# Kernel tuning notes

Measured on AMD Instinct MI355X. Metric: run time of the kernel, lower is better.

Reference implementation:

```python
import jax, jax.numpy as jnp
import numpy as np

B, S, E, D = 4, 2048, 1024, 512


def setup_inputs() -> dict:
    key = jax.random.key(0)
    ks = jax.random.split(key, 7)
    s_in = 1.0 / np.sqrt(E)
    return {
        "x": jax.random.normal(ks[0], (B, S, E), dtype=jnp.float32),
        "wq": jax.random.uniform(ks[1], (E, D), jnp.float32, -s_in, s_in),
        "bq": jax.random.uniform(ks[2], (D,), jnp.float32, -s_in, s_in),
        "wk": jax.random.uniform(ks[3], (E, D), jnp.float32, -s_in, s_in),
        "bk": jax.random.uniform(ks[4], (D,), jnp.float32, -s_in, s_in),
        "wv": jax.random.uniform(ks[5], (E, D), jnp.float32, -s_in, s_in),
        "bv": jax.random.uniform(ks[6], (D,), jnp.float32, -s_in, s_in),
    }


def reference(x, wq, bq, wk, bk, wv, bv):
    # QKV projections: [B,S,E] @ [E,D] -> [B,S,D]
    q = jnp.einsum('bse,ed->bsd', x, wq) + bq
    k = jnp.einsum('bse,ed->bsd', x, wk) + bk
    v = jnp.einsum('bse,ed->bsd', x, wv) + bv
    # scores [B,S,S]
    scores = jnp.einsum('bqd,bkd->bqk', q, k)
    # causal mask applied before scaling (as in original; -inf unaffected by scale)
    causal = jnp.tril(jnp.ones((S, S), dtype=bool))
    scores = jnp.where(causal[None], scores, -jnp.inf)
    scores = scores / jnp.sqrt(jnp.float32(D))
    attn = jax.nn.softmax(scores, axis=-1)
    return jnp.einsum('bqk,bkd->bqd', attn, v)
```

## Files before the change

### kernel.cpp

```cpp
#include <hip/hip_runtime.h>
#include <math.h>


typedef __attribute__((ext_vector_type(4))) float f32x4;
typedef __attribute__((ext_vector_type(16))) float f32x16;
typedef __attribute__((ext_vector_type(8))) short bf16x8;
typedef __attribute__((ext_vector_type(8))) unsigned short u16x8;

#define B_ 4
#define S_ 2048
#define E_ 1024
#define D_ 512

__device__ __forceinline__ unsigned short f2bf(float f) {
  unsigned u = __float_as_uint(f);
  u += 0x7fffu + ((u >> 16) & 1u);
  return (unsigned short)(u >> 16);
}

__device__ __forceinline__ float bf2f(unsigned short h) {
  return __uint_as_float(((unsigned)h) << 16);
}

template<int N> __device__ __forceinline__ void wait_vm() {
  if constexpr (N == 0)      asm volatile("s_waitcnt vmcnt(0)" ::: "memory");
  else if constexpr (N == 3) asm volatile("s_waitcnt vmcnt(3)" ::: "memory");
  else if constexpr (N == 4) asm volatile("s_waitcnt vmcnt(4)" ::: "memory");
  else if constexpr (N == 6) asm volatile("s_waitcnt vmcnt(6)" ::: "memory");
  else static_assert(N != N, "unsupported vmcnt");
}


template<int ROWS, int NTHR>
__device__ __forceinline__ void stage_tile32(const unsigned short* __restrict__ g, long ld,
                                             long rowBase, int kBase,
                                             unsigned short* lds, int tid) {
  constexpr int CALLS = (ROWS * 64) / (NTHR * 16);
  #pragma unroll
  for (int i = 0; i < CALLS; ++i) {
    int idx = i * NTHR + tid;
    int row = idx >> 2, cc = idx & 3;
    int src_g = cc ^ ((row >> 1) & 3);
    __builtin_amdgcn_global_load_lds(
      (const __attribute__((address_space(1))) void*)(g + (rowBase + row) * ld + kBase + src_g * 8),
      (__attribute__((address_space(3))) void*)(lds + idx * 8),
      16, 0, 0);
  }
}

template<int MT, int NTT>
__device__ __forceinline__ void compute_tile32(const unsigned short* As, const unsigned short* Bs,
                                               int a_row0, int b_row0, int lane,
                                               f32x16 (&acc)[MT][NTT]) {
  int lr = lane & 31, lhalf = lane >> 5;
  int p = (lr >> 1) & 3;
  #pragma unroll
  for (int ki = 0; ki < 2; ++ki) {
    int slot = ((ki * 2 + lhalf) ^ p) * 8;
    bf16x8 af[MT], bf[NTT];
    #pragma unroll
    for (int mt = 0; mt < MT; ++mt)
      af[mt] = *(const bf16x8*)(As + (a_row0 + mt * 32 + lr) * 32 + slot);
    #pragma unroll
    for (int nt = 0; nt < NTT; ++nt)
      bf[nt] = *(const bf16x8*)(Bs + (b_row0 + nt * 32 + lr) * 32 + slot);
    #pragma unroll
    for (int mt = 0; mt < MT; ++mt)
      #pragma unroll
      for (int nt = 0; nt < NTT; ++nt)
        acc[mt][nt] = __builtin_amdgcn_mfma_f32_32x32x16_bf16(af[mt], bf[nt], acc[mt][nt], 0, 0, 0);
  }
}

template<int AROWS, int BROWS, int NTHR, int MT, int NTT>
__device__ __forceinline__ void mainloop32(
    const unsigned short* __restrict__ A, long lda, long rowA,
    const unsigned short* __restrict__ Bt, long ldb, long rowB,
    int nsteps, unsigned short* AsBuf, unsigned short* BsBuf,
    int tid, int lane, int a_row0, int b_row0, f32x16 (&acc)[MT][NTT]) {
  constexpr int ASZ = AROWS * 32, BSZ = BROWS * 32;
  constexpr int LPS = (AROWS * 64) / (NTHR * 16) + (BROWS * 64) / (NTHR * 16);
  unsigned short *a0 = AsBuf, *a1 = AsBuf + ASZ, *a2 = AsBuf + 2 * ASZ;
  unsigned short *b0 = BsBuf, *b1 = BsBuf + BSZ, *b2 = BsBuf + 2 * BSZ;
  stage_tile32<AROWS, NTHR>(A, lda, rowA, 0, a0, tid);
  stage_tile32<BROWS, NTHR>(Bt, ldb, rowB, 0, b0, tid);
  if (nsteps > 1) {
    stage_tile32<AROWS, NTHR>(A, lda, rowA, 32, a1, tid);
    stage_tile32<BROWS, NTHR>(Bt, ldb, rowB, 32, b1, tid);
  }
  for (int t = 0; t < nsteps; ++t) {
    if (t < nsteps - 1) wait_vm<LPS>(); else wait_vm<0>();
    __builtin_amdgcn_s_barrier();
    __builtin_amdgcn_sched_barrier(0);
    compute_tile32<MT, NTT>(a0, b0, a_row0, b_row0, lane, acc);
    if (t + 2 < nsteps) {
      stage_tile32<AROWS, NTHR>(A, lda, rowA, (t + 2) * 32, a2, tid);
      stage_tile32<BROWS, NTHR>(Bt, ldb, rowB, (t + 2) * 32, b2, tid);
    }
    unsigned short* ta = a0; a0 = a1; a1 = a2; a2 = ta;
    unsigned short* tb = b0; b0 = b1; b1 = b2; b2 = tb;
  }
}


template<int ROWS, int NTHR>
__device__ __forceinline__ void stage_tile64(const unsigned short* __restrict__ g, long ld,
                                             long rowBase, int kBase,
                                             unsigned short* lds, int tid) {
  constexpr int CALLS = (ROWS * 128) / (NTHR * 16);
  #pragma unroll
  for (int i = 0; i < CALLS; ++i) {
    int idx = i * NTHR + tid;
    int row = idx >> 3, cc = idx & 7;
    int src_g = cc ^ (row & 7);
    __builtin_amdgcn_global_load_lds(
      (const __attribute__((address_space(1))) void*)(g + (rowBase + row) * ld + kBase + src_g * 8),
      (__attribute__((address_space(3))) void*)(lds + idx * 8),
      16, 0, 0);
  }
}

__device__ __forceinline__ void compute_pv64(const unsigned short* As, const unsigned short* Bs,
                                             int a_row0, int b_row0, int lane, bf16x8 ones,
                                             f32x16 (&acc)[2], f32x16& accl) {
  int lr = lane & 31, lhalf = lane >> 5;
  int p = lr & 7;
  #pragma unroll
  for (int ki = 0; ki < 4; ++ki) {
    int slot = ((ki * 2 + lhalf) ^ p) * 8;
    bf16x8 af  = *(const bf16x8*)(As + (a_row0 + lr) * 64 + slot);
    bf16x8 bf0 = *(const bf16x8*)(Bs + (b_row0 + lr) * 64 + slot);
    bf16x8 bf1 = *(const bf16x8*)(Bs + (b_row0 + 32 + lr) * 64 + slot);
    accl   = __builtin_amdgcn_mfma_f32_32x32x16_bf16(af, ones, accl, 0, 0, 0);
    acc[0] = __builtin_amdgcn_mfma_f32_32x32x16_bf16(af, bf0, acc[0], 0, 0, 0);
    acc[1] = __builtin_amdgcn_mfma_f32_32x32x16_bf16(af, bf1, acc[1], 0, 0, 0);
  }
}

__device__ __forceinline__ void pv_mainloop64(
    const unsigned short* __restrict__ A, long rowA,
    const unsigned short* __restrict__ Bt, long rowB,
    int nsteps, unsigned short (*As)[64 * 64], unsigned short (*Bs)[128 * 64],
    int tid, int lane, int a_row0, int b_row0,
    f32x16 (&acc)[2], f32x16& accl) {
  bf16x8 ones;
  #pragma unroll
  for (int j = 0; j < 8; ++j) ones[j] = (short)0x3F80;
  stage_tile64<64, 256>(A, S_, rowA, 0, As[0], tid);
  stage_tile64<128, 256>(Bt, S_, rowB, 0, Bs[0], tid);
  if (nsteps > 1) {
    stage_tile64<64, 256>(A, S_, rowA, 64, As[1], tid);
    stage_tile64<128, 256>(Bt, S_, rowB, 64, Bs[1], tid);
  }
  int cur = 0;
  for (int t = 0; t < nsteps; ++t) {
    if (t < nsteps - 1) wait_vm<6>(); else wait_vm<0>();
    __builtin_amdgcn_s_barrier();
    __builtin_amdgcn_sched_barrier(0);
    compute_pv64(As[cur], Bs[cur], a_row0, b_row0, lane, ones, acc, accl);
    if (t + 2 < nsteps) {
      int nxt = (cur + 2) % 3;
      stage_tile64<64, 256>(A, S_, rowA, (t + 2) * 64, As[nxt], tid);
      stage_tile64<128, 256>(Bt, S_, rowB, (t + 2) * 64, Bs[nxt], tid);
    }
    cur = (cur + 1) % 3;
  }
}


__global__ __launch_bounds__(256) void convert_f32_bf16(const float* __restrict__ src,
                                                        unsigned short* __restrict__ dst) {
  long i = (long)blockIdx.x * 256 + threadIdx.x;
  f32x4 a = ((const f32x4*)src)[2 * i];
  f32x4 b = ((const f32x4*)src)[2 * i + 1];
  u16x8 o;
  #pragma unroll
  for (int j = 0; j < 4; ++j) { o[j] = f2bf(a[j]); o[4 + j] = f2bf(b[j]); }
  ((u16x8*)dst)[i] = o;
}

__global__ __launch_bounds__(256) void build_wT(const float* __restrict__ wq,
                                                const float* __restrict__ wk,
                                                const float* __restrict__ wv,
                                                unsigned short* __restrict__ wbT) {
  int o = blockIdx.x * 256 + threadIdx.x;
  int n = o >> 10, k = o & 1023;
  const float* w = (n < 512) ? wq : ((n < 1024) ? wk : wv);
  int d = n & 511;
  wbT[o] = f2bf(w[(long)k * 512 + d]);
}

__global__ __launch_bounds__(256, 3) void qkv_gemm(
    const unsigned short* __restrict__ xb, const unsigned short* __restrict__ wbT,
    const float* __restrict__ bq, const float* __restrict__ bk, const float* __restrict__ bv,
    unsigned short* __restrict__ qb, unsigned short* __restrict__ kb,
    unsigned short* __restrict__ vb) {
  __shared__ unsigned short As[3][128 * 32], Bs[3][128 * 32];
  int tid = threadIdx.x, wave = tid >> 6, lane = tid & 63;
  int wm = wave >> 1, wn = wave & 1;
  int wg = blockIdx.x;
  int swz = (wg & 7) * 96 + (wg >> 3);
  int nb = swz % 12, mb = swz / 12;
  long rowA = (long)mb * 128, rowB = (long)nb * 128;
  f32x16 acc[2][2] = {};
  mainloop32<128, 128, 256, 2, 2>(xb, E_, rowA, wbT, E_, rowB, E_ / 32,
                                  &As[0][0], &Bs[0][0], tid, lane, wm * 64, wn * 64, acc);
  int lc = lane & 31, lhi = (lane >> 5) * 4;
  #pragma unroll
  for (int nt = 0; nt < 2; ++nt) {
    int n = (int)rowB + wn * 64 + nt * 32 + lc;
    int d = n & 511;
    float bias; unsigned short* dst;
    if (n < 512)       { bias = bq[d]; dst = qb; }
    else if (n < 1024) { bias = bk[d]; dst = kb; }
    else               { bias = bv[d]; dst = vb; }
    #pragma unroll
    for (int mt = 0; mt < 2; ++mt) {
      long mbase = rowA + wm * 64 + mt * 32 + lhi;
      #pragma unroll
      for (int r = 0; r < 16; ++r) {
        long m = mbase + (r & 3) + 8 * (r >> 2);
        dst[m * D_ + d] = f2bf(acc[mt][nt][r] + bias);
      }
    }
  }
}

__global__ __launch_bounds__(256) void transpose_v(const unsigned short* __restrict__ vb,
                                                   unsigned short* __restrict__ vtb) {
  int dblk = blockIdx.x;
  int sblk = blockIdx.y;
  int b = blockIdx.z;
  __shared__ unsigned short ls[64][72];
  int tid = threadIdx.x;
  int r = tid >> 3, c8 = (tid & 7) * 8;
  long d0 = (long)dblk * 64, s0 = (long)sblk * 64;
  #pragma unroll
  for (int p = 0; p < 2; ++p) {
    u16x8 v = *(const u16x8*)(vb + ((long)b * S_ + s0 + r + p * 32) * D_ + d0 + c8);
    *(u16x8*)&ls[r + p * 32][c8] = v;
  }
  __syncthreads();
  #pragma unroll
  for (int p = 0; p < 2; ++p) {
    int d = r + p * 32;
    u16x8 o;
    #pragma unroll
    for (int j = 0; j < 8; ++j) o[j] = ls[c8 + j][d];
    *(u16x8*)(vtb + ((long)b * D_ + d0 + d) * S_ + s0 + c8) = o;
  }
}

__global__ __launch_bounds__(256, 4) void scores_gemm(
    const unsigned short* __restrict__ qb, const unsigned short* __restrict__ kb,
    unsigned short* __restrict__ sc) {
  int jb = blockIdx.x, im = 31 - blockIdx.y, b = blockIdx.z;
  if (2 * jb > im) return;
  __shared__ unsigned short As[3][64 * 32], Bs[3][128 * 32];
  int tid = threadIdx.x, wave = tid >> 6, lane = tid & 63;
  int wm = wave >> 1, wn = wave & 1;
  const unsigned short* A  = qb + (long)b * S_ * D_;
  const unsigned short* Bt = kb + (long)b * S_ * D_;
  long rowA = (long)im * 64, rowB = (long)jb * 128;
  f32x16 acc[1][2] = {};
  mainloop32<64, 128, 256, 1, 2>(A, D_, rowA, Bt, D_, rowB, D_ / 32,
                                 &As[0][0], &Bs[0][0], tid, lane, wm * 32, wn * 64, acc);
  unsigned short* po = sc + (long)b * S_ * S_;
  const float cexp = 1.4426950408889634f / 22.627416997969522f;
  int lc = lane & 31, lhi = (lane >> 5) * 4;
  long mbase = rowA + wm * 32 + lhi;
  #pragma unroll
  for (int r = 0; r < 16; ++r) {
    long m = mbase + (r & 3) + 8 * (r >> 2);
    #pragma unroll
    for (int nt = 0; nt < 2; ++nt) {
      long n = rowB + wn * 64 + nt * 32 + lc;
      float p = (n <= m) ? exp2f(acc[0][nt][r] * cexp) : 0.f;
      po[m * S_ + n] = f2bf(p);
    }
  }
}

__global__ __launch_bounds__(256, 2) void pv_gemm(
    const unsigned short* __restrict__ sc, const unsigned short* __restrict__ vtb,
    float* __restrict__ out) {
  int bn = blockIdx.x, bm = 31 - blockIdx.y, b = blockIdx.z;
  __shared__ unsigned short As[3][64 * 64], Bs[3][128 * 64];
  int tid = threadIdx.x, wave = tid >> 6, lane = tid & 63;
  int wm = wave >> 1, wn = wave & 1;
  const unsigned short* A  = sc  + (long)b * S_ * S_;
  const unsigned short* Bt = vtb + (long)b * D_ * S_;
  long rowA = (long)bm * 64, rowB = (long)bn * 128;
  int nsteps = bm + 1;
  f32x16 acc[2] = {};
  f32x16 accl = {};
  pv_mainloop64(A, rowA, Bt, rowB, nsteps, As, Bs, tid, lane,
                wm * 32, wn * 64, acc, accl);
  float* oo = out + (long)b * S_ * D_;
  int lc = lane & 31, lhi = (lane >> 5) * 4;
  long mbase = rowA + wm * 32 + lhi;
  #pragma unroll
  for (int r = 0; r < 16; ++r) {
    long m = mbase + (r & 3) + 8 * (r >> 2);
    float inv = 1.f / accl[r];
    #pragma unroll
    for (int nt = 0; nt < 2; ++nt) {
      long n = rowB + wn * 64 + nt * 32 + lc;
      oo[m * D_ + n] = acc[nt][r] * inv;
    }
  }
}

extern "C" void kernel_launch(void* const* d_in, const int* in_sizes, int n_in,
                              void* d_out, int out_size, void* d_ws, size_t ws_size,
                              hipStream_t stream) {
  const float* x   = (const float*)d_in[0];
  const float* wq  = (const float*)d_in[1];
  const float* bq  = (const float*)d_in[2];
  const float* wk  = (const float*)d_in[3];
  const float* bk  = (const float*)d_in[4];
  const float* wv  = (const float*)d_in[5];
  const float* bv  = (const float*)d_in[6];
  float* out = (float*)d_out;

  char* ws = (char*)d_ws;
  unsigned short* xb  = (unsigned short*)(ws);
  unsigned short* wbT = (unsigned short*)(ws + 16777216);
  unsigned short* qb  = (unsigned short*)(ws + 19922944);
  unsigned short* kb  = (unsigned short*)(ws + 28311552);
  unsigned short* vb  = (unsigned short*)(ws + 36700160);
  unsigned short* vtb = (unsigned short*)(ws + 45088768);
  unsigned short* sc  = (unsigned short*)(ws + 53477376);

  convert_f32_bf16<<<dim3(4096), dim3(256), 0, stream>>>(x, xb);
  build_wT<<<dim3(6144), dim3(256), 0, stream>>>(wq, wk, wv, wbT);
  qkv_gemm<<<dim3(768), dim3(256), 0, stream>>>(xb, wbT, bq, bk, bv, qb, kb, vb);
  transpose_v<<<dim3(8, 32, 4), dim3(256), 0, stream>>>(vb, vtb);
  scores_gemm<<<dim3(16, 32, 4), dim3(256), 0, stream>>>(qb, kb, sc);
  pv_gemm<<<dim3(4, 32, 4), dim3(256), 0, stream>>>(sc, vtb, out);
}
```

Baseline: 115.9 us.

## Fuse input conversions into one kernel and V transpose into QKV GEMM epilogue

Merges the x bf16 conversion and the weight transpose-convert into a single prep launch. The V-projection blocks of the QKV GEMM now write their tile transposed through LDS straight into the V^T buffer, so the separate transpose kernel and the intermediate V buffer go away. This saves two launches and one full read/write pass over V, at the cost of an extra LDS staging step and barriers in the V epilogue.

```diff
diff --git a/kernel.cpp b/kernel.cpp
--- a/kernel.cpp
+++ b/kernel.cpp
@@ -168,34 +168,38 @@
 }
 
 
-__global__ __launch_bounds__(256) void convert_f32_bf16(const float* __restrict__ src,
-                                                        unsigned short* __restrict__ dst) {
-  long i = (long)blockIdx.x * 256 + threadIdx.x;
-  f32x4 a = ((const f32x4*)src)[2 * i];
-  f32x4 b = ((const f32x4*)src)[2 * i + 1];
-  u16x8 o;
-  #pragma unroll
-  for (int j = 0; j < 4; ++j) { o[j] = f2bf(a[j]); o[4 + j] = f2bf(b[j]); }
-  ((u16x8*)dst)[i] = o;
-}
-
-__global__ __launch_bounds__(256) void build_wT(const float* __restrict__ wq,
-                                                const float* __restrict__ wk,
-                                                const float* __restrict__ wv,
-                                                unsigned short* __restrict__ wbT) {
-  int o = blockIdx.x * 256 + threadIdx.x;
-  int n = o >> 10, k = o & 1023;
-  const float* w = (n < 512) ? wq : ((n < 1024) ? wk : wv);
-  int d = n & 511;
-  wbT[o] = f2bf(w[(long)k * 512 + d]);
+__global__ __launch_bounds__(256) void prep(const float* __restrict__ x,
+                                            const float* __restrict__ wq,
+                                            const float* __restrict__ wk,
+                                            const float* __restrict__ wv,
+                                            unsigned short* __restrict__ xb,
+                                            unsigned short* __restrict__ wbT) {
+  int bx = blockIdx.x;
+  if (bx < 4096) {
+    long i = (long)bx * 256 + threadIdx.x;
+    f32x4 a = ((const f32x4*)x)[2 * i];
+    f32x4 b = ((const f32x4*)x)[2 * i + 1];
+    u16x8 o;
+    #pragma unroll
+    for (int j = 0; j < 4; ++j) { o[j] = f2bf(a[j]); o[4 + j] = f2bf(b[j]); }
+    ((u16x8*)xb)[i] = o;
+  } else {
+    int o = (bx - 4096) * 256 + threadIdx.x;
+    int n = o >> 10, k = o & 1023;
+    const float* w = (n < 512) ? wq : ((n < 1024) ? wk : wv);
+    int d = n & 511;
+    wbT[o] = f2bf(w[(long)k * 512 + d]);
+  }
 }
 
 __global__ __launch_bounds__(256, 3) void qkv_gemm(
     const unsigned short* __restrict__ xb, const unsigned short* __restrict__ wbT,
     const float* __restrict__ bq, const float* __restrict__ bk, const float* __restrict__ bv,
     unsigned short* __restrict__ qb, unsigned short* __restrict__ kb,
-    unsigned short* __restrict__ vb) {
-  __shared__ unsigned short As[3][128 * 32], Bs[3][128 * 32];
+    unsigned short* __restrict__ vtb) {
+  __shared__ unsigned short lds[24576];
+  unsigned short* AsB = lds;
+  unsigned short* BsB = lds + 3 * 4096;
   int tid = threadIdx.x, wave = tid >> 6, lane = tid & 63;
   int wm = wave >> 1, wn = wave & 1;
   int wg = blockIdx.x;
@@ -204,50 +208,51 @@
   long rowA = (long)mb * 128, rowB = (long)nb * 128;
   f32x16 acc[2][2] = {};
   mainloop32<128, 128, 256, 2, 2>(xb, E_, rowA, wbT, E_, rowB, E_ / 32,
-                                  &As[0][0], &Bs[0][0], tid, lane, wm * 64, wn * 64, acc);
+                                  AsB, BsB, tid, lane, wm * 64, wn * 64, acc);
   int lc = lane & 31, lhi = (lane >> 5) * 4;
-  #pragma unroll
-  for (int nt = 0; nt < 2; ++nt) {
-    int n = (int)rowB + wn * 64 + nt * 32 + lc;
-    int d = n & 511;
-    float bias; unsigned short* dst;
-    if (n < 512)       { bias = bq[d]; dst = qb; }
-    else if (n < 1024) { bias = bk[d]; dst = kb; }
-    else               { bias = bv[d]; dst = vb; }
-    #pragma unroll
-    for (int mt = 0; mt < 2; ++mt) {
-      long mbase = rowA + wm * 64 + mt * 32 + lhi;
+  if (rowB < 1024) {
+    #pragma unroll
+    for (int nt = 0; nt < 2; ++nt) {
+      int n = (int)rowB + wn * 64 + nt * 32 + lc;
+      int d = n & 511;
+      float bias; unsigned short* dst;
+      if (n < 512) { bias = bq[d]; dst = qb; }
+      else         { bias = bk[d]; dst = kb; }
       #pragma unroll
-      for (int r = 0; r < 16; ++r) {
-        long m = mbase + (r & 3) + 8 * (r >> 2);
-        dst[m * D_ + d] = f2bf(acc[mt][nt][r] + bias);
+      for (int mt = 0; mt < 2; ++mt) {
+        long mbase = rowA + wm * 64 + mt * 32 + lhi;
+        #pragma unroll
+        for (int r = 0; r < 16; ++r) {
+          long m = mbase + (r & 3) + 8 * (r >> 2);
+          dst[m * D_ + d] = f2bf(acc[mt][nt][r] + bias);
+        }
       }
     }
-  }
-}
-
-__global__ __launch_bounds__(256) void transpose_v(const unsigned short* __restrict__ vb,
-                                                   unsigned short* __restrict__ vtb) {
-  int dblk = blockIdx.x;
-  int sblk = blockIdx.y;
-  int b = blockIdx.z;
-  __shared__ unsigned short ls[64][72];
-  int tid = threadIdx.x;
-  int r = tid >> 3, c8 = (tid & 7) * 8;
-  long d0 = (long)dblk * 64, s0 = (long)sblk * 64;
-  #pragma unroll
-  for (int p = 0; p < 2; ++p) {
-    u16x8 v = *(const u16x8*)(vb + ((long)b * S_ + s0 + r + p * 32) * D_ + d0 + c8);
-    *(u16x8*)&ls[r + p * 32][c8] = v;
-  }
-  __syncthreads();
-  #pragma unroll
-  for (int p = 0; p < 2; ++p) {
-    int d = r + p * 32;
-    u16x8 o;
-    #pragma unroll
-    for (int j = 0; j < 8; ++j) o[j] = ls[c8 + j][d];
-    *(u16x8*)(vtb + ((long)b * D_ + d0 + d) * S_ + s0 + c8) = o;
+  } else {
+    __syncthreads();
+    #pragma unroll
+    for (int nt = 0; nt < 2; ++nt) {
+      int n_loc = wn * 64 + nt * 32 + lc;
+      float bias = bv[(int)(rowB - 1024) + n_loc];
+      #pragma unroll
+      for (int mt = 0; mt < 2; ++mt) {
+        int mb0 = wm * 64 + mt * 32 + lhi;
+        #pragma unroll
+        for (int r = 0; r < 16; ++r) {
+          int m_loc = mb0 + (r & 3) + 8 * (r >> 2);
+          lds[n_loc * 136 + m_loc] = f2bf(acc[mt][nt][r] + bias);
+        }
+      }
+    }
+    __syncthreads();
+    int d_loc = tid >> 1, hf = tid & 1;
+    long d = (rowB - 1024) + d_loc;
+    long bb = rowA >> 11;
+    long s0 = (rowA & 2047) + hf * 64;
+    unsigned short* dstv = vtb + (bb * D_ + d) * (long)S_ + s0;
+    #pragma unroll
+    for (int j = 0; j < 8; ++j)
+      *(u16x8*)(dstv + j * 8) = *(const u16x8*)&lds[d_loc * 136 + hf * 64 + j * 8];
   }
 }
 
@@ -328,14 +333,11 @@
   unsigned short* wbT = (unsigned short*)(ws + 16777216);
   unsigned short* qb  = (unsigned short*)(ws + 19922944);
   unsigned short* kb  = (unsigned short*)(ws + 28311552);
-  unsigned short* vb  = (unsigned short*)(ws + 36700160);
-  unsigned short* vtb = (unsigned short*)(ws + 45088768);
-  unsigned short* sc  = (unsigned short*)(ws + 53477376);
-
-  convert_f32_bf16<<<dim3(4096), dim3(256), 0, stream>>>(x, xb);
-  build_wT<<<dim3(6144), dim3(256), 0, stream>>>(wq, wk, wv, wbT);
-  qkv_gemm<<<dim3(768), dim3(256), 0, stream>>>(xb, wbT, bq, bk, bv, qb, kb, vb);
-  transpose_v<<<dim3(8, 32, 4), dim3(256), 0, stream>>>(vb, vtb);
+  unsigned short* vtb = (unsigned short*)(ws + 36700160);
+  unsigned short* sc  = (unsigned short*)(ws + 45088768);
+
+  prep<<<dim3(10240), dim3(256), 0, stream>>>(x, wq, wk, wv, xb, wbT);
+  qkv_gemm<<<dim3(768), dim3(256), 0, stream>>>(xb, wbT, bq, bk, bv, qb, kb, vtb);
   scores_gemm<<<dim3(16, 32, 4), dim3(256), 0, stream>>>(qb, kb, sc);
   pv_gemm<<<dim3(4, 32, 4), dim3(256), 0, stream>>>(sc, vtb, out);
 }
```

Measured after the change: 109.3 us. -5.7%, faster.
